# Optimization experiments

Hardware: AMD Instinct MI355X
Metric: run time of the kernel (lower is better)

Reference implementation:

```python
import jax, jax.numpy as jnp
import numpy as np

HEADS = 16


def setup_inputs() -> dict:
    key = jax.random.key(0)
    ks = jax.random.split(key, 6)
    B, S, D = 2, 2048, 1024
    return {
        "x": jax.random.normal(ks[0], (B, S, D), dtype=jnp.float32),
        "q_in": jax.random.normal(ks[1], (B, S, D), dtype=jnp.float32),
        "WQ": jax.random.normal(ks[2], (D, D), dtype=jnp.float32) * 0.03,
        "WK": jax.random.normal(ks[3], (D, D), dtype=jnp.float32) * 0.03,
        "WV": jax.random.normal(ks[4], (D, D), dtype=jnp.float32) * 0.03,
        "WO": jax.random.normal(ks[5], (D, D), dtype=jnp.float32) * 0.03,
    }


def reference(x, q_in, WQ, WK, WV, WO):
    B, S, D = x.shape
    H = HEADS
    hd = D // H
    # projections; tf.split on last dim == reshape to (B,S,H,hd)
    Q = (q_in @ WQ).reshape(B, S, H, hd)
    K = (x @ WK).reshape(B, S, H, hd)
    V = (x @ WV).reshape(B, S, H, hd)
    scores = jnp.einsum("bqhd,bkhd->bhqk", Q, K)  # [B,H,S,S]
    # causal additive mask: 0 on/below diagonal, -inf above
    causal = jnp.tril(jnp.ones((S, S), dtype=bool))
    mask = jnp.where(causal, 0.0, -jnp.inf).astype(scores.dtype)
    # NOTE: original adds the mask BEFORE scaling, and scales by sqrt(d_model)
    attn = jax.nn.softmax((scores + mask) / np.sqrt(D).astype(scores.dtype), axis=-1)
    ctx = jnp.einsum("bhqk,bkhd->bqhd", attn, V).reshape(B, S, D)
    return ctx @ WO
```

## Files before the change

kernel.cpp:

```cpp
#include <hip/hip_runtime.h>


typedef __bf16 bf16_t;
typedef __attribute__((ext_vector_type(8))) __bf16 bf16x8;
typedef __attribute__((ext_vector_type(4))) __bf16 bf16x4;
typedef __attribute__((ext_vector_type(4))) float f32x4;

#define SCALE_LOG2E 0.045084220027780106f
#define FIXED_MAX 8.0f

__device__ __forceinline__ void async_load16(const void* g, void* l) {
  __builtin_amdgcn_global_load_lds(
      (const __attribute__((address_space(1))) void*)g,
      (__attribute__((address_space(3))) void*)l, 16, 0, 0);
}

__global__ void prep(const float* __restrict__ x, const float* __restrict__ q,
                     const float* __restrict__ w0, const float* __restrict__ w1,
                     const float* __restrict__ w2, const float* __restrict__ w3,
                     bf16_t* __restrict__ xb, bf16_t* __restrict__ qb,
                     bf16_t* __restrict__ wt) {
  const int bid = blockIdx.x;
  if (bid < 4096) {
    const float* src = (bid >= 2048) ? q : x;
    bf16_t* dst = (bid >= 2048) ? qb : xb;
    const size_t i = ((size_t)(bid & 2047) * 256 + threadIdx.x) * 8;
    float4 v0 = *(const float4*)(src + i);
    float4 v1 = *(const float4*)(src + i + 4);
    bf16x8 o;
    o[0] = (bf16_t)v0.x; o[1] = (bf16_t)v0.y; o[2] = (bf16_t)v0.z; o[3] = (bf16_t)v0.w;
    o[4] = (bf16_t)v1.x; o[5] = (bf16_t)v1.y; o[6] = (bf16_t)v1.z; o[7] = (bf16_t)v1.w;
    *(bf16x8*)(dst + i) = o;
  } else {
    const int wb = bid - 4096;
    const int z = wb >> 8;
    const float* W = z == 0 ? w0 : z == 1 ? w1 : z == 2 ? w2 : w3;
    bf16_t* dst = wt + (size_t)z * 1048576;
    const int r0 = ((wb >> 4) & 15) * 64, c0 = (wb & 15) * 64;
    __shared__ bf16_t t[64][72];
#pragma unroll
    for (int i = 0; i < 16; ++i) {
      int flat = i * 256 + threadIdx.x;
      int r = flat >> 6, c = flat & 63;
      t[c][r] = (bf16_t)W[(size_t)(r0 + r) * 1024 + c0 + c];
    }
    __syncthreads();
    const int c = threadIdx.x >> 2, seg = (threadIdx.x & 3) * 16;
    bf16x8 a = *(const bf16x8*)&t[c][seg];
    bf16x8 b = *(const bf16x8*)&t[c][seg + 8];
    bf16_t* drow = dst + (size_t)(c0 + c) * 1024 + r0 + seg;
    *(bf16x8*)drow = a;
    *(bf16x8*)(drow + 8) = b;
  }
}

template <int MODE>
__global__ __launch_bounds__(256, MODE == 2 ? 4 : 3) void gemm128(
    const bf16_t* __restrict__ Aq, const bf16_t* __restrict__ Ax,
    const bf16_t* __restrict__ Bt,
    bf16_t* __restrict__ Cq, bf16_t* __restrict__ Cvt, float* __restrict__ Cf) {
  constexpr int K = 1024;
  constexpr int NT = (MODE == 2) ? 2 : 4;
  constexpr int NROWS = NT * 32;
  const int n0 = blockIdx.x * NROWS;
  const int m0 = blockIdx.y * 128;
  const bf16_t* A = (MODE == 0 && n0 >= 1024) ? Ax : Aq;

  __shared__ bf16_t lA[128 * 64];
  __shared__ bf16_t lB[NROWS * 64];

  const int tid = threadIdx.x;
  const int w = tid >> 6, l = tid & 63;
  const int wm = (w & 1) * 64, wn = (w >> 1) * (NT * 16);
  const int fr = l & 15, fq = l >> 4;
  const int xr = fr & 7;
  const int srow = l >> 3;
  const int swz = ((l & 7) ^ srow) * 8;

  const int gk0 = (fq ^ xr) * 8;
  const int gk1 = ((4 + fq) ^ xr) * 8;

  f32x4 acc[4][NT] = {};

  for (int kt = 0; kt < K; kt += 64) {
    __syncthreads();
#pragma unroll
    for (int c = 0; c < 4; ++c) {
      const int ch = w * 4 + c;
      async_load16(A + (size_t)(m0 + ch * 8 + srow) * K + kt + swz, &lA[ch * 512]);
      if (NT == 4) {
        async_load16(Bt + (size_t)(n0 + ch * 8 + srow) * K + kt + swz, &lB[ch * 512]);
      } else if (c < 2) {
        const int bch = w * 2 + c;
        async_load16(Bt + (size_t)(n0 + bch * 8 + srow) * K + kt + swz, &lB[bch * 512]);
      }
    }
    __syncthreads();
    bf16x8 af[4][2], bfr[NT][2];
#pragma unroll
    for (int i = 0; i < 4; ++i) {
      const int row = (wm + i * 16 + fr) * 64;
      af[i][0] = *(const bf16x8*)&lA[row + gk0];
      af[i][1] = *(const bf16x8*)&lA[row + gk1];
    }
#pragma unroll
    for (int j = 0; j < NT; ++j) {
      const int row = (wn + j * 16 + fr) * 64;
      bfr[j][0] = *(const bf16x8*)&lB[row + gk0];
      bfr[j][1] = *(const bf16x8*)&lB[row + gk1];
    }
#pragma unroll
    for (int i = 0; i < 4; ++i)
#pragma unroll
      for (int j = 0; j < NT; ++j) {
        acc[i][j] = __builtin_amdgcn_mfma_f32_16x16x32_bf16(af[i][0], bfr[j][0], acc[i][j], 0, 0, 0);
        acc[i][j] = __builtin_amdgcn_mfma_f32_16x16x32_bf16(af[i][1], bfr[j][1], acc[i][j], 0, 0, 0);
      }
  }

  if (MODE == 2) {
#pragma unroll
    for (int i = 0; i < 4; ++i) {
      const int m = m0 + wm + i * 16 + fq * 4;
#pragma unroll
      for (int j = 0; j < NT; ++j) {
        const int n = n0 + wn + j * 16 + fr;
#pragma unroll
        for (int r = 0; r < 4; ++r) Cf[(size_t)(m + r) * 1024 + n] = acc[i][j][r];
      }
    }
  } else if (n0 < 2048) {
#pragma unroll
    for (int i = 0; i < 4; ++i) {
      const int m = m0 + wm + i * 16 + fq * 4;
#pragma unroll
      for (int j = 0; j < NT; ++j) {
        const int n = n0 + wn + j * 16 + fr;
#pragma unroll
        for (int r = 0; r < 4; ++r) Cq[(size_t)(m + r) * 3072 + n] = (bf16_t)acc[i][j][r];
      }
    }
  } else {
#pragma unroll
    for (int i = 0; i < 4; ++i) {
      const int mb = m0 + wm + i * 16 + fq * 4;
      const int bb = mb >> 11, ss = mb & 2047;
#pragma unroll
      for (int j = 0; j < NT; ++j) {
        const int nn = n0 - 2048 + wn + j * 16 + fr;
        const int hh = nn >> 6, dd = nn & 63;
        bf16x4 pk;
#pragma unroll
        for (int r = 0; r < 4; ++r) pk[r] = (bf16_t)acc[i][j][r];
        *(bf16x4*)(Cvt + (size_t)((bb * 16 + hh) * 64 + dd) * 2048 + ss) = pk;
      }
    }
  }
}

__global__ __launch_bounds__(512, 4) void attn8w(const bf16_t* __restrict__ qkv,
                                                 const bf16_t* __restrict__ vt,
                                                 bf16_t* __restrict__ ctx) {
  const int lin = blockIdx.x;
  const int swzb = ((lin & 7) << 6) | (lin >> 3);
  const int p = swzb & 15;
  const int bh = swzb >> 4;
  const int b = bh >> 4, h = bh & 15;
  const int tid = threadIdx.x, w = tid >> 6, l = tid & 63;
  const int fr = l & 15, fq = l >> 4;
  const int qq4 = w & 3;
  const int kh = w >> 2;

  __shared__ __align__(16) bf16_t lK[2][64 * 64];
  __shared__ __align__(16) bf16_t lV[2][64 * 64];
  __shared__ __align__(16) bf16_t lP[8][16 * 40];
  __shared__ __align__(16) float lRed[4][16][68];

  const bf16_t* kg = qkv + (size_t)b * 2048 * 3072 + 1024 + h * 64;
  const bf16_t* vg = vt + (size_t)(b * 16 + h) * 64 * 2048;

  const int srow = l >> 3;
  const int swz = ((l & 7) ^ srow) * 8;
  const int xr = fr & 7;

  const int kbase = (kh * 32 + fr) * 64;
  const int g0 = (fq ^ xr) * 8, g1 = ((4 + fq) ^ xr) * 8;
  const int vbase = fr * 64;
  const int vg0 = ((kh * 4 + fq) ^ xr) * 8;
  const int pwr = fr * 40 + fq * 4;
  const int prd = fr * 40 + fq * 8;
  bf16_t* lPw = &lP[w][0];

  bf16x8 ones;
#pragma unroll
  for (int i = 0; i < 8; ++i) ones[i] = (bf16_t)1.0f;

#pragma unroll 1
  for (int phase = 0; phase < 2; ++phase) {
    const int qt = (phase == 0) ? (16 + p) : (15 - p);
    const int qw = qt * 64 + qq4 * 16;

    bf16x8 qf[2];
#pragma unroll
    for (int ks = 0; ks < 2; ++ks)
      qf[ks] = *(const bf16x8*)(qkv + (size_t)(b * 2048 + qw + fr) * 3072 +
                                h * 64 + ks * 32 + fq * 8);

    f32x4 o[4] = {};
    f32x4 liacc = {};

    const bf16_t* kp = kg + (size_t)(w * 8 + srow) * 3072 + swz;
    const bf16_t* vp = vg + (size_t)(w * 8 + srow) * 2048 + swz;

    if (phase == 1) __syncthreads();
    async_load16(kp, &lK[0][w * 512]);
    async_load16(vp, &lV[0][w * 512]);
    kp += 64 * 3072;
    vp += 64;

    auto compute = [&](int kt, int buf) {
      const int kb = kt * 64 + kh * 32;
      if (kb > qw + 15) return;
      const bf16_t* lKb = &lK[buf][0];
      const bf16_t* lVb = &lV[buf][0];
      f32x4 s[2] = {};
      __builtin_amdgcn_s_setprio(1);
#pragma unroll
      for (int t = 0; t < 2; ++t) {
        bf16x8 k0 = *(const bf16x8*)&lKb[kbase + t * 1024 + g0];
        bf16x8 k1 = *(const bf16x8*)&lKb[kbase + t * 1024 + g1];
        s[t] = __builtin_amdgcn_mfma_f32_16x16x32_bf16(k0, qf[0], s[t], 0, 0, 0);
        s[t] = __builtin_amdgcn_mfma_f32_16x16x32_bf16(k1, qf[1], s[t], 0, 0, 0);
      }
      __builtin_amdgcn_s_setprio(0);
      const int qq = qw + fr;
      const bool needmask = (kb + 31) > qw;
#pragma unroll
      for (int t = 0; t < 2; ++t) {
        bf16x4 pk;
#pragma unroll
        for (int r = 0; r < 4; ++r) {
          float v = fmaf(s[t][r], SCALE_LOG2E, -FIXED_MAX);
          if (needmask && (kb + t * 16 + fq * 4 + r > qq)) v = -1e30f;
          pk[r] = (bf16_t)__builtin_amdgcn_exp2f(v);
        }
        *(bf16x4*)&lPw[pwr + t * 16] = pk;
      }
      bf16x8 pf = *(const bf16x8*)&lPw[prd];
      __builtin_amdgcn_s_setprio(1);
#pragma unroll
      for (int dt = 0; dt < 4; ++dt) {
        bf16x8 vf = *(const bf16x8*)&lVb[vbase + dt * 1024 + vg0];
        o[dt] = __builtin_amdgcn_mfma_f32_16x16x32_bf16(vf, pf, o[dt], 0, 0, 0);
      }
      liacc = __builtin_amdgcn_mfma_f32_16x16x32_bf16(ones, pf, liacc, 0, 0, 0);
      __builtin_amdgcn_s_setprio(0);
    };

    int kt = 0;
#pragma unroll 1
    while (true) {
      __syncthreads();
      if (kt < qt) {
        async_load16(kp, &lK[1][w * 512]);
        async_load16(vp, &lV[1][w * 512]);
        kp += 64 * 3072; vp += 64;
      }
      compute(kt, 0);
      if (++kt > qt) break;
      __syncthreads();
      if (kt < qt) {
        async_load16(kp, &lK[0][w * 512]);
        async_load16(vp, &lV[0][w * 512]);
        kp += 64 * 3072; vp += 64;
      }
      compute(kt, 1);
      if (++kt > qt) break;
    }

    __syncthreads();
    if (kh) {
#pragma unroll
      for (int dt = 0; dt < 4; ++dt)
        *(f32x4*)&lRed[qq4][fr][dt * 16 + fq * 4] = o[dt];
      if (fq == 0) lRed[qq4][fr][64] = liacc[0];
    }
    __syncthreads();
    if (!kh) {
      const float lsum = liacc[0] + lRed[qq4][fr][64];
      const float inv = 1.f / lsum;
      bf16_t* cb = ctx + (size_t)(b * 2048 + qw + fr) * 1024 + h * 64;
#pragma unroll
      for (int dt = 0; dt < 4; ++dt) {
        f32x4 v = o[dt] + *(f32x4*)&lRed[qq4][fr][dt * 16 + fq * 4];
        bf16x4 ov;
#pragma unroll
        for (int r = 0; r < 4; ++r) ov[r] = (bf16_t)(v[r] * inv);
        *(bf16x4*)(cb + dt * 16 + fq * 4) = ov;
      }
    }
  }
}

extern "C" void kernel_launch(void* const* d_in, const int* in_sizes, int n_in,
                              void* d_out, int out_size, void* d_ws, size_t ws_size,
                              hipStream_t stream) {
  const float* x  = (const float*)d_in[0];
  const float* q  = (const float*)d_in[1];
  const float* WQ = (const float*)d_in[2];
  const float* WK = (const float*)d_in[3];
  const float* WV = (const float*)d_in[4];
  const float* WO = (const float*)d_in[5];
  float* out = (float*)d_out;

  bf16_t* qb  = (bf16_t*)d_ws;
  bf16_t* xb  = qb + 4194304;
  bf16_t* wt  = xb + 4194304;
  bf16_t* qkv = wt + 4194304;
  bf16_t* vtp = qkv + (size_t)4096 * 3072;
  bf16_t* ctx = vtp + 4194304;

  prep<<<dim3(5120), 256, 0, stream>>>(x, q, WQ, WK, WV, WO, xb, qb, wt);
  gemm128<0><<<dim3(24, 32), 256, 0, stream>>>(qb, xb, wt, qkv, vtp, nullptr);
  attn8w<<<dim3(512), 512, 0, stream>>>(qkv, vtp, ctx);
  gemm128<2><<<dim3(16, 32), 256, 0, stream>>>(ctx, ctx, wt + (size_t)3072 * 1024,
                                               nullptr, nullptr, out);
}
```

Baseline: 185.1 us.

## Use 128-row query tiles per block with longest-first scheduling

Each attention block now handles one 128-row query tile, with each wave holding two 16-row query slices, instead of pairing a 64-row tile with its causal mirror across two phases. Each K/V tile loaded into LDS is reused for twice as many query rows, which halves K/V traffic and barrier count per query row. Blocks are ordered so the longest causal tiles launch first, for load balance. The grid must change to 512 blocks, and the larger P buffer plus doubled accumulators raise LDS and register pressure at 4 blocks per CU.

```diff
diff --git a/kernel.cpp b/kernel.cpp
--- a/kernel.cpp
+++ b/kernel.cpp
@@ -161,10 +161,9 @@
 __global__ __launch_bounds__(512, 4) void attn8w(const bf16_t* __restrict__ qkv,
                                                  const bf16_t* __restrict__ vt,
                                                  bf16_t* __restrict__ ctx) {
-  const int lin = blockIdx.x;
-  const int swzb = ((lin & 7) << 6) | (lin >> 3);
-  const int p = swzb & 15;
-  const int bh = swzb >> 4;
+  const int bid = blockIdx.x;
+  const int qt = 15 - (bid >> 5);
+  const int bh = bid & 31;
   const int b = bh >> 4, h = bh & 15;
   const int tid = threadIdx.x, w = tid >> 6, l = tid & 63;
   const int fr = l & 15, fq = l >> 4;
@@ -173,7 +172,7 @@
 
   __shared__ __align__(16) bf16_t lK[2][64 * 64];
   __shared__ __align__(16) bf16_t lV[2][64 * 64];
-  __shared__ __align__(16) bf16_t lP[8][16 * 40];
+  __shared__ __align__(16) bf16_t lP[8][32 * 40];
   __shared__ __align__(16) float lRed[4][16][68];
 
   const bf16_t* kg = qkv + (size_t)b * 2048 * 3072 + 1024 + h * 64;
@@ -187,112 +186,124 @@
   const int g0 = (fq ^ xr) * 8, g1 = ((4 + fq) ^ xr) * 8;
   const int vbase = fr * 64;
   const int vg0 = ((kh * 4 + fq) ^ xr) * 8;
-  const int pwr = fr * 40 + fq * 4;
-  const int prd = fr * 40 + fq * 8;
   bf16_t* lPw = &lP[w][0];
 
+  const int qw = qt * 128 + qq4 * 32;
+  const int nkt = 2 * qt + 2;
+
   bf16x8 ones;
 #pragma unroll
   for (int i = 0; i < 8; ++i) ones[i] = (bf16_t)1.0f;
 
-#pragma unroll 1
-  for (int phase = 0; phase < 2; ++phase) {
-    const int qt = (phase == 0) ? (16 + p) : (15 - p);
-    const int qw = qt * 64 + qq4 * 16;
-
-    bf16x8 qf[2];
+  bf16x8 qf[2][2];
+#pragma unroll
+  for (int qs = 0; qs < 2; ++qs)
 #pragma unroll
     for (int ks = 0; ks < 2; ++ks)
-      qf[ks] = *(const bf16x8*)(qkv + (size_t)(b * 2048 + qw + fr) * 3072 +
-                                h * 64 + ks * 32 + fq * 8);
-
-    f32x4 o[4] = {};
-    f32x4 liacc = {};
-
-    const bf16_t* kp = kg + (size_t)(w * 8 + srow) * 3072 + swz;
-    const bf16_t* vp = vg + (size_t)(w * 8 + srow) * 2048 + swz;
-
-    if (phase == 1) __syncthreads();
-    async_load16(kp, &lK[0][w * 512]);
-    async_load16(vp, &lV[0][w * 512]);
-    kp += 64 * 3072;
-    vp += 64;
-
-    auto compute = [&](int kt, int buf) {
-      const int kb = kt * 64 + kh * 32;
-      if (kb > qw + 15) return;
-      const bf16_t* lKb = &lK[buf][0];
-      const bf16_t* lVb = &lV[buf][0];
-      f32x4 s[2] = {};
-      __builtin_amdgcn_s_setprio(1);
-#pragma unroll
-      for (int t = 0; t < 2; ++t) {
-        bf16x8 k0 = *(const bf16x8*)&lKb[kbase + t * 1024 + g0];
-        bf16x8 k1 = *(const bf16x8*)&lKb[kbase + t * 1024 + g1];
-        s[t] = __builtin_amdgcn_mfma_f32_16x16x32_bf16(k0, qf[0], s[t], 0, 0, 0);
-        s[t] = __builtin_amdgcn_mfma_f32_16x16x32_bf16(k1, qf[1], s[t], 0, 0, 0);
-      }
-      __builtin_amdgcn_s_setprio(0);
-      const int qq = qw + fr;
-      const bool needmask = (kb + 31) > qw;
+      qf[qs][ks] = *(const bf16x8*)(qkv + (size_t)(b * 2048 + qw + qs * 16 + fr) * 3072 +
+                                    h * 64 + ks * 32 + fq * 8);
+
+  f32x4 o[2][4] = {};
+  f32x4 li[2] = {};
+
+  const bf16_t* kp = kg + (size_t)(w * 8 + srow) * 3072 + swz;
+  const bf16_t* vp = vg + (size_t)(w * 8 + srow) * 2048 + swz;
+
+  async_load16(kp, &lK[0][w * 512]);
+  async_load16(vp, &lV[0][w * 512]);
+  kp += 64 * 3072;
+  vp += 64;
+
+  auto compute = [&](int kt, int buf) {
+    const int kb = kt * 64 + kh * 32;
+    if (kb > qw + 31) return;
+    const bf16_t* lKb = &lK[buf][0];
+    const bf16_t* lVb = &lV[buf][0];
+    f32x4 s[2][2] = {};
+    __builtin_amdgcn_s_setprio(1);
+#pragma unroll
+    for (int t = 0; t < 2; ++t) {
+      bf16x8 k0 = *(const bf16x8*)&lKb[kbase + t * 1024 + g0];
+      bf16x8 k1 = *(const bf16x8*)&lKb[kbase + t * 1024 + g1];
+#pragma unroll
+      for (int qs = 0; qs < 2; ++qs) {
+        s[qs][t] = __builtin_amdgcn_mfma_f32_16x16x32_bf16(k0, qf[qs][0], s[qs][t], 0, 0, 0);
+        s[qs][t] = __builtin_amdgcn_mfma_f32_16x16x32_bf16(k1, qf[qs][1], s[qs][t], 0, 0, 0);
+      }
+    }
+    __builtin_amdgcn_s_setprio(0);
+#pragma unroll
+    for (int qs = 0; qs < 2; ++qs) {
+      const int qq = qw + qs * 16 + fr;
+      const bool needmask = (kb + 31) > (qw + qs * 16);
 #pragma unroll
       for (int t = 0; t < 2; ++t) {
         bf16x4 pk;
 #pragma unroll
         for (int r = 0; r < 4; ++r) {
-          float v = fmaf(s[t][r], SCALE_LOG2E, -FIXED_MAX);
+          float v = fmaf(s[qs][t][r], SCALE_LOG2E, -FIXED_MAX);
           if (needmask && (kb + t * 16 + fq * 4 + r > qq)) v = -1e30f;
           pk[r] = (bf16_t)__builtin_amdgcn_exp2f(v);
         }
-        *(bf16x4*)&lPw[pwr + t * 16] = pk;
-      }
-      bf16x8 pf = *(const bf16x8*)&lPw[prd];
-      __builtin_amdgcn_s_setprio(1);
+        *(bf16x4*)&lPw[(qs * 16 + fr) * 40 + fq * 4 + t * 16] = pk;
+      }
+    }
+    bf16x8 pf[2];
+#pragma unroll
+    for (int qs = 0; qs < 2; ++qs)
+      pf[qs] = *(const bf16x8*)&lPw[(qs * 16 + fr) * 40 + fq * 8];
+    __builtin_amdgcn_s_setprio(1);
+#pragma unroll
+    for (int dt = 0; dt < 4; ++dt) {
+      bf16x8 vf = *(const bf16x8*)&lVb[vbase + dt * 1024 + vg0];
+#pragma unroll
+      for (int qs = 0; qs < 2; ++qs)
+        o[qs][dt] = __builtin_amdgcn_mfma_f32_16x16x32_bf16(vf, pf[qs], o[qs][dt], 0, 0, 0);
+    }
+#pragma unroll
+    for (int qs = 0; qs < 2; ++qs)
+      li[qs] = __builtin_amdgcn_mfma_f32_16x16x32_bf16(ones, pf[qs], li[qs], 0, 0, 0);
+    __builtin_amdgcn_s_setprio(0);
+  };
+
+  int kt = 0;
+#pragma unroll 1
+  while (true) {
+    __syncthreads();
+    if (kt + 1 < nkt) {
+      async_load16(kp, &lK[1][w * 512]);
+      async_load16(vp, &lV[1][w * 512]);
+      kp += 64 * 3072; vp += 64;
+    }
+    compute(kt, 0);
+    if (++kt >= nkt) break;
+    __syncthreads();
+    if (kt + 1 < nkt) {
+      async_load16(kp, &lK[0][w * 512]);
+      async_load16(vp, &lV[0][w * 512]);
+      kp += 64 * 3072; vp += 64;
+    }
+    compute(kt, 1);
+    if (++kt >= nkt) break;
+  }
+
+#pragma unroll 1
+  for (int qs = 0; qs < 2; ++qs) {
+    __syncthreads();
+    if (kh) {
+#pragma unroll
+      for (int dt = 0; dt < 4; ++dt)
+        *(f32x4*)&lRed[qq4][fr][dt * 16 + fq * 4] = o[qs][dt];
+      if (fq == 0) lRed[qq4][fr][64] = li[qs][0];
+    }
+    __syncthreads();
+    if (!kh) {
+      const float lsum = li[qs][0] + lRed[qq4][fr][64];
+      const float inv = 1.f / lsum;
+      bf16_t* cb = ctx + (size_t)(b * 2048 + qw + qs * 16 + fr) * 1024 + h * 64;
 #pragma unroll
       for (int dt = 0; dt < 4; ++dt) {
-        bf16x8 vf = *(const bf16x8*)&lVb[vbase + dt * 1024 + vg0];
-        o[dt] = __builtin_amdgcn_mfma_f32_16x16x32_bf16(vf, pf, o[dt], 0, 0, 0);
-      }
-      liacc = __builtin_amdgcn_mfma_f32_16x16x32_bf16(ones, pf, liacc, 0, 0, 0);
-      __builtin_amdgcn_s_setprio(0);
-    };
-
-    int kt = 0;
-#pragma unroll 1
-    while (true) {
-      __syncthreads();
-      if (kt < qt) {
-        async_load16(kp, &lK[1][w * 512]);
-        async_load16(vp, &lV[1][w * 512]);
-        kp += 64 * 3072; vp += 64;
-      }
-      compute(kt, 0);
-      if (++kt > qt) break;
-      __syncthreads();
-      if (kt < qt) {
-        async_load16(kp, &lK[0][w * 512]);
-        async_load16(vp, &lV[0][w * 512]);
-        kp += 64 * 3072; vp += 64;
-      }
-      compute(kt, 1);
-      if (++kt > qt) break;
-    }
-
-    __syncthreads();
-    if (kh) {
-#pragma unroll
-      for (int dt = 0; dt < 4; ++dt)
-        *(f32x4*)&lRed[qq4][fr][dt * 16 + fq * 4] = o[dt];
-      if (fq == 0) lRed[qq4][fr][64] = liacc[0];
-    }
-    __syncthreads();
-    if (!kh) {
-      const float lsum = liacc[0] + lRed[qq4][fr][64];
-      const float inv = 1.f / lsum;
-      bf16_t* cb = ctx + (size_t)(b * 2048 + qw + fr) * 1024 + h * 64;
-#pragma unroll
-      for (int dt = 0; dt < 4; ++dt) {
-        f32x4 v = o[dt] + *(f32x4*)&lRed[qq4][fr][dt * 16 + fq * 4];
+        f32x4 v = o[qs][dt] + *(f32x4*)&lRed[qq4][fr][dt * 16 + fq * 4];
         bf16x4 ov;
 #pragma unroll
         for (int r = 0; r < 4; ++r) ov[r] = (bf16_t)(v[r] * inv);
```

New measurement: 394.1 us. 113% more time.
